# Kernel tuning notes

Hardware: AMD Instinct MI355X
Metric: run time of the kernel (lower is better)

## Reference

```python
import jax, jax.numpy as jnp
import numpy as np

HEADS = 8
DIM_HEAD = 64
SCALE = DIM_HEAD ** -0.5

def setup_inputs() -> dict:
    key = jax.random.key(0)
    k1, k2, k3 = jax.random.split(key, 3)
    B, N, D = 4, 2048, 512
    inner = HEADS * DIM_HEAD  # 512
    x = jax.random.normal(k1, (B, N, D), dtype=jnp.float32)
    w_qkv = jax.random.normal(k2, (D, inner * 3), dtype=jnp.float32) * (D ** -0.5)
    w_out = jax.random.normal(k3, (inner, D), dtype=jnp.float32) * (inner ** -0.5)
    b_out = jnp.zeros((D,), dtype=jnp.float32)
    return {"x": x, "w_qkv": w_qkv, "w_out": w_out, "b_out": b_out}

def reference(x, w_qkv, w_out, b_out):
    B, N, D = x.shape
    qkv = x @ w_qkv  # [B, N, 3*inner]
    q, k, v = jnp.split(qkv, 3, axis=-1)
    # b n (h d) -> b h n d
    def to_heads(t):
        return t.reshape(B, N, HEADS, DIM_HEAD).transpose(0, 2, 1, 3)
    q, k, v = to_heads(q), to_heads(k), to_heads(v)
    dots = jnp.einsum('bhid,bhjd->bhij', q, k) * SCALE  # [B,H,N,N]
    attn = jax.nn.softmax(dots, axis=-1)
    out = jnp.einsum('bhij,bhjd->bhid', attn, v)  # [B,H,N,Dh]
    out = out.transpose(0, 2, 1, 3).reshape(B, N, HEADS * DIM_HEAD)
    return out @ w_out + b_out
```

## Files before the change

kernel.cpp:

```cpp
#include <hip/hip_runtime.h>
#include <hip/hip_bf16.h>
#include <math.h>
#include <stdint.h>


typedef unsigned short u16;
typedef __attribute__((ext_vector_type(4))) float f32x4;
typedef __attribute__((ext_vector_type(8))) short bf16x8;
typedef __attribute__((ext_vector_type(4))) short s16x4;

#define AS1 __attribute__((address_space(1)))
#define AS3 __attribute__((address_space(3)))
#define MFMA(a, b, c) __builtin_amdgcn_mfma_f32_16x16x32_bf16(a, b, c, 0, 0, 0)
#define QSCALE 0.180336880f

__device__ __forceinline__ u16 f2bf(float f) {
  union { float f; unsigned u; } v; v.f = f;
  unsigned r = v.u + 0x7FFFu + ((v.u >> 16) & 1u);
  return (u16)(r >> 16);
}
__device__ __forceinline__ float bf2f(u16 b) {
  union { unsigned u; float f; } v; v.u = ((unsigned)b) << 16; return v.f;
}
__device__ __forceinline__ void gld16(const u16* g, u16* l) {
  __builtin_amdgcn_global_load_lds((const AS1 void*)g, (AS3 void*)l, 16, 0, 0);
}
__device__ __forceinline__ float u2f(unsigned u) {
  union { unsigned u; float f; } v; v.u = u; return v.f;
}
__device__ __forceinline__ unsigned f2u(float f) {
  union { float f; unsigned u; } v; v.f = f; return v.u;
}
__device__ __forceinline__ int cvtpk(float lo, float hi) {
  int r; asm("v_cvt_pk_bf16_f32 %0, %1, %2" : "=v"(r) : "v"(lo), "v"(hi));
  return r;
}
__device__ __forceinline__ float fexp2(float x) {
  float r; asm("v_exp_f32 %0, %1" : "=v"(r) : "v"(x));
  return r;
}

__global__ void k_cast(const float* __restrict__ s, u16* __restrict__ h, int n) {
  int i = (blockIdx.x * 256 + threadIdx.x) * 4;
  if (i < n) {
    f32x4 v = *(const f32x4*)&s[i];
    s16x4 hh;
    #pragma unroll
    for (int j = 0; j < 4; ++j) hh[j] = (short)f2bf(v[j]);
    *(s16x4*)&h[i] = hh;
  }
}

__global__ void k_tcast(const float* __restrict__ s, u16* __restrict__ h,
                        int N, int total) {
  int i = blockIdx.x * 256 + threadIdx.x;
  if (i < total) {
    int n = i >> 9, k = i & 511;
    h[i] = f2bf(s[(size_t)k * N + n]);
  }
}

__device__ __forceinline__ void gemm_core(
    const u16* __restrict__ Ah, const u16* __restrict__ Bh,
    char* sm, int rowA, int rowB, int tid, f32x4 (&acc)[4][4]) {
  const int wid = tid >> 6, lane = tid & 63;
  const int x = lane & 15, h = lane >> 4;
  const int wr = wid >> 1, wc = wid & 1;
  const int d0 = wid * 1024 + lane * 16;
  const int lg0 = d0 ^ (((d0 >> 7) & 7) << 4);
  const int srow = lg0 >> 6;
  const int scol = (lg0 & 63) >> 1;
  const int swk = ((lane >> 1) & 7) << 4;
  const char* smA = sm + (((wr * 64 + x) * 64 + h * 16) ^ swk);
  const char* smB = sm + (((wc * 64 + x) * 64 + h * 16) ^ swk);

  for (int kt = 0; kt < 16; ++kt) {
    const int kofs = kt * 32;
    __syncthreads();
    #pragma unroll
    for (int r = 0; r < 2; ++r) {
      const int row  = r * 64 + srow;
      const int ldst = r * 4096 + wid * 1024;
      const size_t ga = (size_t)(rowA + row) * 512 + kofs + scol;
      const size_t gb = (size_t)(rowB + row) * 512 + kofs + scol;
      gld16(Ah + ga, (u16*)(sm + ldst));
      gld16(Bh + gb, (u16*)(sm + 16384 + ldst));
    }
    __syncthreads();
    bf16x8 a_h[4], b_h[4];
    #pragma unroll
    for (int i = 0; i < 4; ++i)
      a_h[i] = *(const bf16x8*)(smA + i * 1024);
    #pragma unroll
    for (int j = 0; j < 4; ++j)
      b_h[j] = *(const bf16x8*)(smB + 16384 + j * 1024);
    __builtin_amdgcn_s_setprio(1);
    #pragma unroll
    for (int i = 0; i < 4; ++i)
      #pragma unroll
      for (int j = 0; j < 4; ++j)
        acc[i][j] = MFMA(a_h[i], b_h[j], acc[i][j]);
    __builtin_amdgcn_s_setprio(0);
  }
}

__global__ __launch_bounds__(256) void k_gemm_qkv(
    const u16* __restrict__ Ah, const u16* __restrict__ Bh,
    u16* __restrict__ Qb, u16* __restrict__ Kb, u16* __restrict__ Vt) {
  __shared__ __align__(1024) char sm[32768];
  const int tid = threadIdx.x, lane = tid & 63, wid = tid >> 6;
  const int x = lane & 15, h = lane >> 4;
  const int wr = wid >> 1, wc = wid & 1;
  const int rowA = blockIdx.x * 128, rowB = blockIdx.y * 128;
  f32x4 acc[4][4] = {};
  gemm_core(Ah, Bh, sm, rowA, rowB, tid, acc);

  #pragma unroll
  for (int i = 0; i < 4; ++i)
    #pragma unroll
    for (int j = 0; j < 4; ++j) {
      const int n = rowB + wc * 64 + j * 16 + x;
      const int which = n >> 9;
      const int hh = (n >> 6) & 7, d = n & 63;
      const int m0 = rowA + wr * 64 + i * 16 + h * 4;
      const int b = m0 >> 11, is0 = m0 & 2047;
      if (which == 0) {
        #pragma unroll
        for (int r = 0; r < 4; ++r) {
          const size_t idx = ((size_t)((b * 8 + hh) * 2048 + is0 + r)) * 64 + d;
          Qb[idx] = f2bf(acc[i][j][r] * QSCALE);
        }
      } else if (which == 1) {
        #pragma unroll
        for (int r = 0; r < 4; ++r) {
          const size_t idx = ((size_t)((b * 8 + hh) * 2048 + is0 + r)) * 64 + d;
          Kb[idx] = f2bf(acc[i][j][r]);
        }
      } else {
        s16x4 vv;
        #pragma unroll
        for (int r = 0; r < 4; ++r) vv[r] = (short)f2bf(acc[i][j][r]);
        *(s16x4*)&Vt[((size_t)((b * 8 + hh) * 64 + d)) * 2048 + is0] = vv;
      }
    }
}

__global__ __launch_bounds__(256) void k_gemm_out(
    const u16* __restrict__ Ah, const u16* __restrict__ Bh,
    const float* __restrict__ bias, float* __restrict__ out) {
  __shared__ __align__(1024) char sm[32768];
  const int tid = threadIdx.x, lane = tid & 63, wid = tid >> 6;
  const int x = lane & 15, h = lane >> 4;
  const int wr = wid >> 1, wc = wid & 1;
  const int rowA = blockIdx.x * 128, rowB = blockIdx.y * 128;
  f32x4 acc[4][4] = {};
  gemm_core(Ah, Bh, sm, rowA, rowB, tid, acc);

  #pragma unroll
  for (int i = 0; i < 4; ++i)
    #pragma unroll
    for (int j = 0; j < 4; ++j) {
      const int n = rowB + wc * 64 + j * 16 + x;
      #pragma unroll
      for (int r = 0; r < 4; ++r) {
        const int m = rowA + wr * 64 + i * 16 + h * 4 + r;
        out[(size_t)m * 512 + n] = acc[i][j][r] + bias[n];
      }
    }
}

__global__ __launch_bounds__(512, 2) void k_attn(
    const u16* __restrict__ Qb,
    const u16* __restrict__ Kb, const u16* __restrict__ Vt,
    u16* __restrict__ OP,
    float* __restrict__ Mm,
    float* __restrict__ Sm) {
  __shared__ __align__(1024) char sm[65536];
  const int tid = threadIdx.x, wid = tid >> 6, lane = tid & 63;
  const int x = lane & 15, h = lane >> 4;

  const int fid = blockIdx.x;
  const int l = (fid & 7) * 64 + (fid >> 3);
  const int half = l & 1, qb = (l >> 1) & 7, bh = l >> 4;

  const size_t base = (size_t)bh * 2048 * 64;
  const int qr0 = qb * 256 + wid * 32;
  const size_t kv0 = (size_t)half * 1024;

  bf16x8 qh[2][2];
  #pragma unroll
  for (int g = 0; g < 2; ++g) {
    const size_t rq = base + (size_t)(qr0 + g * 16 + x) * 64 + h * 8;
    #pragma unroll
    for (int ks = 0; ks < 2; ++ks)
      qh[g][ks] = *(const bf16x8*)&Qb[rq + ks * 32];
  }

  bf16x8 ones;
  #pragma unroll
  for (int j = 0; j < 8; ++j) ones[j] = (short)0x3F80;

  const int db = tid * 16;
  const int lg = db ^ (((db >> 7) & 7) << 4);
  const int sks  = db >> 12;
  const int srow = (lg >> 6) & 63;
  const int scb  = (lg & 63) >> 1;
  const size_t offK = (size_t)srow * 64 + sks * 32 + scb;
  const size_t offV = (size_t)srow * 2048 + sks * 32 + scb;

  const int swk = ((lane >> 1) & 7) << 4;
  const int rdo = (x * 64 + h * 16) ^ swk;
  char* const pb = sm + 32768 + wid * 4096;
  const int pxor = (x & 7) << 4;
  const int prow = x * 128;

  float mrun[2] = {-INFINITY, -INFINITY};
  f32x4 o[2][4] = {};
  f32x4 os[2] = {};

  {
    gld16(Kb + base + kv0 * 64 + offK, (u16*)(sm + db));
    gld16(Vt + base + kv0 + offV,      (u16*)(sm + 8192 + db));
  }

  for (int kv = 0; kv < 16; ++kv) {
    const int bb = (kv & 1) * 16384;
    __builtin_amdgcn_s_barrier();
    if (kv < 15) {
      const size_t kvb = kv0 + (size_t)(kv + 1) * 64;
      char* buf = sm + (16384 - bb);
      gld16(Kb + base + kvb * 64 + offK, (u16*)(buf + db));
      gld16(Vt + base + kvb + offV,      (u16*)(buf + 8192 + db));
      asm volatile("s_waitcnt vmcnt(2)" ::: "memory");
    } else {
      asm volatile("s_waitcnt vmcnt(0)" ::: "memory");
    }
    __builtin_amdgcn_s_barrier();

    const char* smb = sm + bb + rdo;

    f32x4 s[2][4] = {};
    __builtin_amdgcn_s_setprio(1);
    #pragma unroll
    for (int c = 0; c < 4; ++c)
      #pragma unroll
      for (int ks = 0; ks < 2; ++ks) {
        bf16x8 kb_ = *(const bf16x8*)(smb + ks * 4096 + c * 1024);
        s[0][c] = MFMA(kb_, qh[0][ks], s[0][c]);
        s[1][c] = MFMA(kb_, qh[1][ks], s[1][c]);
      }
    __builtin_amdgcn_s_setprio(0);

    float pm[2];
    #pragma unroll
    for (int g = 0; g < 2; ++g) {
      float m0 = fmaxf(fmaxf(s[g][0][0], s[g][0][1]), s[g][0][2]);
      float m1 = fmaxf(fmaxf(s[g][0][3], s[g][1][0]), s[g][1][1]);
      float m2 = fmaxf(fmaxf(s[g][1][2], s[g][1][3]), s[g][2][0]);
      float m3 = fmaxf(fmaxf(s[g][2][1], s[g][2][2]), s[g][2][3]);
      float m4 = fmaxf(fmaxf(s[g][3][0], s[g][3][1]), s[g][3][2]);
      float m5 = fmaxf(fmaxf(m0, m1), m2);
      float p  = fmaxf(fmaxf(fmaxf(m3, m4), s[g][3][3]), m5);
      p = fmaxf(p, __shfl_xor(p, 16, 64));
      p = fmaxf(p, __shfl_xor(p, 32, 64));
      pm[g] = p;
    }

    if (__any((pm[0] > mrun[0] + 7.0f) || (pm[1] > mrun[1] + 7.0f))) {
      #pragma unroll
      for (int g = 0; g < 2; ++g) {
        float mnew = fmaxf(mrun[g], pm[g]);
        float scl = fexp2(mrun[g] - mnew);
        mrun[g] = mnew;
        #pragma unroll
        for (int r = 0; r < 4; ++r) {
          float sq = u2f((unsigned)__builtin_amdgcn_ds_bpermute(
              (20 * h + r) * 4, (int)f2u(scl)));
          os[g][r] *= sq;
          #pragma unroll
          for (int dg = 0; dg < 4; ++dg) o[g][dg][r] *= sq;
        }
      }
    }

    #pragma unroll
    for (int g = 0; g < 2; ++g)
      #pragma unroll
      for (int c = 0; c < 4; ++c) {
        int w0 = cvtpk(fexp2(s[g][c][0] - mrun[g]),
                       fexp2(s[g][c][1] - mrun[g]));
        int w1 = cvtpk(fexp2(s[g][c][2] - mrun[g]),
                       fexp2(s[g][c][3] - mrun[g]));
        int* dst = (int*)(pb + g * 2048 + prow + ((c * 32 + h * 8) ^ pxor));
        dst[0] = w0; dst[1] = w1;
      }

    __builtin_amdgcn_s_setprio(1);
    #pragma unroll
    for (int ch = 0; ch < 2; ++ch) {
      bf16x8 pa0 = *(const bf16x8*)(pb + prow +
                                    ((ch * 64 + h * 16) ^ pxor));
      bf16x8 pa1 = *(const bf16x8*)(pb + 2048 + prow +
                                    ((ch * 64 + h * 16) ^ pxor));
      os[0] = MFMA(pa0, ones, os[0]);
      os[1] = MFMA(pa1, ones, os[1]);
      #pragma unroll
      for (int dg = 0; dg < 4; ++dg) {
        bf16x8 vb = *(const bf16x8*)(smb + 8192 + ch * 4096 + dg * 1024);
        o[0][dg] = MFMA(pa0, vb, o[0][dg]);
        o[1][dg] = MFMA(pa1, vb, o[1][dg]);
      }
    }
    __builtin_amdgcn_s_setprio(0);
  }

  u16* op = OP + (size_t)half * 4194304 + ((size_t)(bh * 2048 + qr0)) * 64;
  #pragma unroll
  for (int g = 0; g < 2; ++g) {
    #pragma unroll
    for (int r = 0; r < 4; ++r) {
      const int row = g * 16 + h * 4 + r;
      #pragma unroll
      for (int dg = 0; dg < 4; ++dg)
        op[(size_t)row * 64 + dg * 16 + x] = f2bf(o[g][dg][r]);
      if (x == 0)
        Sm[half * 65536 + bh * 2048 + qr0 + g * 16 + h * 4 + r] = os[g][r];
    }
    if (h == 0)
      Mm[half * 65536 + bh * 2048 + qr0 + g * 16 + x] = mrun[g];
  }
}

__global__ __launch_bounds__(256) void k_combine(
    const u16* __restrict__ OP, const float* __restrict__ Mm,
    const float* __restrict__ Sm, u16* __restrict__ AO) {
  const int gi = blockIdx.x * 256 + threadIdx.x;
  const int d4 = (gi & 15) * 4;
  const int rb = gi >> 4;
  const float m1 = Mm[rb], m2 = Mm[65536 + rb];
  const float s1 = Sm[rb], s2 = Sm[65536 + rb];
  const float m = fmaxf(m1, m2);
  const float a1 = fexp2(m1 - m), a2 = fexp2(m2 - m);
  const float inv = 1.0f / (s1 * a1 + s2 * a2);
  const float w1 = a1 * inv, w2 = a2 * inv;
  s16x4 p1 = *(const s16x4*)&OP[(size_t)rb * 64 + d4];
  s16x4 p2 = *(const s16x4*)&OP[4194304 + (size_t)rb * 64 + d4];
  const int bh = rb >> 11, row = rb & 2047;
  const int b = bh >> 3, head = bh & 7;
  s16x4 r_;
  #pragma unroll
  for (int j = 0; j < 4; ++j)
    r_[j] = (short)f2bf(bf2f((u16)p1[j]) * w1 + bf2f((u16)p2[j]) * w2);
  *(s16x4*)&AO[((size_t)(b * 2048 + row)) * 512 + head * 64 + d4] = r_;
}

extern "C" void kernel_launch(void* const* d_in, const int* in_sizes, int n_in,
                              void* d_out, int out_size, void* d_ws, size_t ws_size,
                              hipStream_t stream) {
  const float* x    = (const float*)d_in[0];
  const float* wqkv = (const float*)d_in[1];
  const float* wout = (const float*)d_in[2];
  const float* bout = (const float*)d_in[3];
  float* out = (float*)d_out;

  char* w = (char*)d_ws;
  u16* xh  = (u16*)(w + 0);
  u16* wqh = (u16*)(w + 16777216);
  u16* woh = (u16*)(w + 19922944);
  u16* Qb  = (u16*)(w + 20971520);
  u16* Kb  = (u16*)(w + 37748736);
  u16* Vt  = (u16*)(w + 46137344);
  u16* AO  = (u16*)(w + 54525952);
  u16*   OP = (u16*)(w + 0);
  float* Mm = (float*)(w + 16777216);
  float* Sm = (float*)(w + 17301504);

  k_cast <<<4096, 256, 0, stream>>>(x, xh, 4194304);
  k_tcast<<<3072, 256, 0, stream>>>(wqkv, wqh, 1536, 786432);
  k_tcast<<<1024, 256, 0, stream>>>(wout, woh, 512, 262144);
  k_gemm_qkv<<<dim3(64, 12), 256, 0, stream>>>(xh, wqh, Qb, Kb, Vt);
  k_attn<<<512, 512, 0, stream>>>(Qb, Kb, Vt, OP, Mm, Sm);
  k_combine<<<4096, 256, 0, stream>>>(OP, Mm, Sm, AO);
  k_gemm_out<<<dim3(64, 4), 256, 0, stream>>>(AO, woh, bout, out);
}
```

Measured before the change: 106.7 us.

## Double-buffer LDS tiles in GEMM core to prefetch next k-tile

The GEMM main loop now keeps two LDS buffers. It issues the direct-to-LDS global loads for tile kt+1 while tile kt is consumed, and uses explicit vmcnt waits with raw s_barrier instead of __syncthreads. This is meant to hide global load latency behind the MFMA work. The risk is correctness: the vmcnt counts are hand-tuned and s_barrier does not wait on LDS, so ordering and hazards must hold.

New measurement: 96.46 us. 9.6% less time.

```diff
diff --git a/kernel.cpp b/kernel.cpp
--- a/kernel.cpp
+++ b/kernel.cpp
@@ -66,34 +66,50 @@
   const int wid = tid >> 6, lane = tid & 63;
   const int x = lane & 15, h = lane >> 4;
   const int wr = wid >> 1, wc = wid & 1;
-  const int d0 = wid * 1024 + lane * 16;
+  const int d0 = tid * 16;
   const int lg0 = d0 ^ (((d0 >> 7) & 7) << 4);
   const int srow = lg0 >> 6;
   const int scol = (lg0 & 63) >> 1;
   const int swk = ((lane >> 1) & 7) << 4;
-  const char* smA = sm + (((wr * 64 + x) * 64 + h * 16) ^ swk);
-  const char* smB = sm + (((wc * 64 + x) * 64 + h * 16) ^ swk);
+  const int rdoA = ((wr * 64 + x) * 64 + h * 16) ^ swk;
+  const int rdoB = (((wc * 64 + x) * 64 + h * 16) ^ swk) + 8192;
+
+  {
+    #pragma unroll
+    for (int r = 0; r < 2; ++r) {
+      const size_t ga = (size_t)(rowA + r * 64 + srow) * 512 + scol;
+      const size_t gb = (size_t)(rowB + r * 64 + srow) * 512 + scol;
+      gld16(Ah + ga, (u16*)(sm + r * 4096 + d0));
+      gld16(Bh + gb, (u16*)(sm + 8192 + r * 4096 + d0));
+    }
+  }
 
   for (int kt = 0; kt < 16; ++kt) {
-    const int kofs = kt * 32;
-    __syncthreads();
-    #pragma unroll
-    for (int r = 0; r < 2; ++r) {
-      const int row  = r * 64 + srow;
-      const int ldst = r * 4096 + wid * 1024;
-      const size_t ga = (size_t)(rowA + row) * 512 + kofs + scol;
-      const size_t gb = (size_t)(rowB + row) * 512 + kofs + scol;
-      gld16(Ah + ga, (u16*)(sm + ldst));
-      gld16(Bh + gb, (u16*)(sm + 16384 + ldst));
-    }
-    __syncthreads();
+    const int bb = (kt & 1) * 16384;
+    __builtin_amdgcn_s_barrier();
+    if (kt < 15) {
+      const int kofs = (kt + 1) * 32;
+      char* buf = sm + (16384 - bb);
+      #pragma unroll
+      for (int r = 0; r < 2; ++r) {
+        const size_t ga = (size_t)(rowA + r * 64 + srow) * 512 + kofs + scol;
+        const size_t gb = (size_t)(rowB + r * 64 + srow) * 512 + kofs + scol;
+        gld16(Ah + ga, (u16*)(buf + r * 4096 + d0));
+        gld16(Bh + gb, (u16*)(buf + 8192 + r * 4096 + d0));
+      }
+      asm volatile("s_waitcnt vmcnt(4)" ::: "memory");
+    } else {
+      asm volatile("s_waitcnt vmcnt(0)" ::: "memory");
+    }
+    __builtin_amdgcn_s_barrier();
+
     bf16x8 a_h[4], b_h[4];
     #pragma unroll
     for (int i = 0; i < 4; ++i)
-      a_h[i] = *(const bf16x8*)(smA + i * 1024);
+      a_h[i] = *(const bf16x8*)(sm + bb + rdoA + i * 1024);
     #pragma unroll
     for (int j = 0; j < 4; ++j)
-      b_h[j] = *(const bf16x8*)(smB + 16384 + j * 1024);
+      b_h[j] = *(const bf16x8*)(sm + bb + rdoB + j * 1024);
     __builtin_amdgcn_s_setprio(1);
     #pragma unroll
     for (int i = 0; i < 4; ++i)
```
